# Performance work log

Hardware: AMD Instinct MI355X
Metric: run time of the kernel (lower is better)

The kernel has to match this reference:

```python
import jax, jax.numpy as jnp
import numpy as np

K = 4  # kernel_size

def setup_inputs() -> dict:
    key = jax.random.key(0)
    k1, k2, k3 = jax.random.split(key, 3)
    B, T, C = 4, 4096, 2048
    x = jax.random.normal(k1, (B, T, C), dtype=jnp.float32)
    # depthwise Conv1d weight (C, 1, K) flattened to (C, K); PyTorch default init scale
    bound = 1.0 / np.sqrt(K)
    weight = jax.random.uniform(k2, (C, K), dtype=jnp.float32, minval=-bound, maxval=bound)
    bias = jax.random.uniform(k3, (C,), dtype=jnp.float32, minval=-bound, maxval=bound)
    return {"x": x, "weight": weight, "bias": bias}

def reference(x, weight, bias):
    # Causal depthwise conv on (B,T,C) directly (no transpose needed in jax):
    # y[b,t,c] = sum_k weight[c,k] * x[b, t-(K-1)+k, c] + bias[c]; out = x + y
    B, T, C = x.shape
    xp = jnp.pad(x, ((0, 0), (K - 1, 0), (0, 0)))  # left-pad time axis
    y = bias[None, None, :]
    for k in range(K):  # small fixed kernel taps
        y = y + xp[:, k:k + T, :] * weight[None, None, :, k]
    return x + y
```

## Files before the change

kernel.cpp:

```cpp
#include <hip/hip_runtime.h>

#define B_DIM 4
#define T_DIM 4096
#define C_DIM 2048
#define KK 4
#define C4 (C_DIM / 4)
#define ROWS (B_DIM * T_DIM)
#define NV4 (ROWS * C4)
#define BLOCK 256
#define NBLK 2048
#define NTHREADS (NBLK * BLOCK)
#define ITERS (NV4 / NTHREADS)

typedef float v4f __attribute__((ext_vector_type(4)));

__global__ __launch_bounds__(256) void canonconv_kernel(
    const float* __restrict__ x,
    const float* __restrict__ w,
    const float* __restrict__ bias,
    float* __restrict__ out)
{
    const int tid = blockIdx.x * BLOCK + threadIdx.x;
    const int c4  = tid & (C4 - 1);
    const int c   = c4 * 4;

    const v4f* wv = (const v4f*)(w + (size_t)c * KK);
    const v4f a0 = wv[0];
    const v4f a1 = wv[1];
    const v4f a2 = wv[2];
    const v4f a3 = wv[3];
    const v4f bv = *(const v4f*)(bias + c);

    v4f tap0, tap1, tap2, tap3;
    tap0.x = a0.x; tap0.y = a1.x; tap0.z = a2.x; tap0.w = a3.x;
    tap1.x = a0.y; tap1.y = a1.y; tap1.z = a2.y; tap1.w = a3.y;
    tap2.x = a0.z; tap2.y = a1.z; tap2.z = a2.z; tap2.w = a3.z;
    tap3.x = 1.0f + a0.w; tap3.y = 1.0f + a1.w; tap3.z = 1.0f + a2.w; tap3.w = 1.0f + a3.w;

    const v4f* xv = (const v4f*)x;
    v4f*       ov = (v4f*)out;

    #pragma unroll 1
    for (int iter = 0; iter < ITERS; ++iter) {
        const int p   = tid + iter * NTHREADS;
        const int row = p >> 9;
        const int t   = row & (T_DIM - 1);

        const v4f xc = xv[p];
        v4f xm1 = (v4f)0.0f, xm2 = (v4f)0.0f, xm3 = (v4f)0.0f;
        if (t >= 1) xm1 = xv[p - C4];
        if (t >= 2) xm2 = xv[p - 2 * C4];
        if (t >= 3) xm3 = xv[p - 3 * C4];

        v4f r;
        r.x = fmaf(xc.x, tap3.x, fmaf(xm1.x, tap2.x, fmaf(xm2.x, tap1.x, fmaf(xm3.x, tap0.x, bv.x))));
        r.y = fmaf(xc.y, tap3.y, fmaf(xm1.y, tap2.y, fmaf(xm2.y, tap1.y, fmaf(xm3.y, tap0.y, bv.y))));
        r.z = fmaf(xc.z, tap3.z, fmaf(xm1.z, tap2.z, fmaf(xm2.z, tap1.z, fmaf(xm3.z, tap0.z, bv.z))));
        r.w = fmaf(xc.w, tap3.w, fmaf(xm1.w, tap2.w, fmaf(xm2.w, tap1.w, fmaf(xm3.w, tap0.w, bv.w))));

        ov[p] = r;
    }
}

extern "C" void kernel_launch(void* const* d_in, const int* in_sizes, int n_in,
                              void* d_out, int out_size, void* d_ws, size_t ws_size,
                              hipStream_t stream) {
    const float* x    = (const float*)d_in[0];
    const float* w    = (const float*)d_in[1];
    const float* bias = (const float*)d_in[2];
    float* out = (float*)d_out;

    canonconv_kernel<<<NBLK, BLOCK, 0, stream>>>(x, w, bias, out);
}
```

Baseline: 255.1 us.

## Tile rows per block and reuse previous time steps in registers

Each block now handles 16 consecutive time rows for all 512 channel vectors. Each thread keeps a sliding window of the last three inputs in registers instead of reloading them from global memory. This cuts redundant loads, roughly four reads per output down to one plus a three-row halo per tile, and removes per-element boundary branches. In exchange the grid changes to 1024 blocks of 512 threads with a fully unrolled loop, which raises register use and changes occupancy.

New measurement: 237.0 us. -7.1%, faster.

```diff
diff --git a/kernel.cpp b/kernel.cpp
--- a/kernel.cpp
+++ b/kernel.cpp
@@ -6,23 +6,22 @@
 #define KK 4
 #define C4 (C_DIM / 4)
 #define ROWS (B_DIM * T_DIM)
-#define NV4 (ROWS * C4)
-#define BLOCK 256
-#define NBLK 2048
-#define NTHREADS (NBLK * BLOCK)
-#define ITERS (NV4 / NTHREADS)
+#define BLOCK 512
+#define RR 16
+#define NBLK (ROWS / RR)
 
 typedef float v4f __attribute__((ext_vector_type(4)));
 
-__global__ __launch_bounds__(256) void canonconv_kernel(
+__global__ __launch_bounds__(512) void canonconv_kernel(
     const float* __restrict__ x,
     const float* __restrict__ w,
     const float* __restrict__ bias,
     float* __restrict__ out)
 {
-    const int tid = blockIdx.x * BLOCK + threadIdx.x;
-    const int c4  = tid & (C4 - 1);
-    const int c   = c4 * 4;
+    const int c4   = threadIdx.x;
+    const int row0 = blockIdx.x * RR;
+    const int t0   = row0 & (T_DIM - 1);
+    const int c    = c4 * 4;
 
     const v4f* wv = (const v4f*)(w + (size_t)c * KK);
     const v4f a0 = wv[0];
@@ -37,28 +36,32 @@
     tap2.x = a0.z; tap2.y = a1.z; tap2.z = a2.z; tap2.w = a3.z;
     tap3.x = 1.0f + a0.w; tap3.y = 1.0f + a1.w; tap3.z = 1.0f + a2.w; tap3.w = 1.0f + a3.w;
 
-    const v4f* xv = (const v4f*)x;
-    v4f*       ov = (v4f*)out;
+    const v4f* xp = (const v4f*)x + (size_t)row0 * C4 + c4;
+    v4f*       op = (v4f*)out     + (size_t)row0 * C4 + c4;
 
-    #pragma unroll 1
-    for (int iter = 0; iter < ITERS; ++iter) {
-        const int p   = tid + iter * NTHREADS;
-        const int row = p >> 9;
-        const int t   = row & (T_DIM - 1);
+    v4f xm1, xm2, xm3;
+    if (t0 != 0) {
+        xm3 = xp[-3 * C4];
+        xm2 = xp[-2 * C4];
+        xm1 = xp[-1 * C4];
+    } else {
+        xm3 = (v4f)0.0f;
+        xm2 = (v4f)0.0f;
+        xm1 = (v4f)0.0f;
+    }
 
-        const v4f xc = xv[p];
-        v4f xm1 = (v4f)0.0f, xm2 = (v4f)0.0f, xm3 = (v4f)0.0f;
-        if (t >= 1) xm1 = xv[p - C4];
-        if (t >= 2) xm2 = xv[p - 2 * C4];
-        if (t >= 3) xm3 = xv[p - 3 * C4];
-
+    #pragma unroll
+    for (int j = 0; j < RR; ++j) {
+        const v4f xc = xp[j * C4];
         v4f r;
         r.x = fmaf(xc.x, tap3.x, fmaf(xm1.x, tap2.x, fmaf(xm2.x, tap1.x, fmaf(xm3.x, tap0.x, bv.x))));
         r.y = fmaf(xc.y, tap3.y, fmaf(xm1.y, tap2.y, fmaf(xm2.y, tap1.y, fmaf(xm3.y, tap0.y, bv.y))));
         r.z = fmaf(xc.z, tap3.z, fmaf(xm1.z, tap2.z, fmaf(xm2.z, tap1.z, fmaf(xm3.z, tap0.z, bv.z))));
         r.w = fmaf(xc.w, tap3.w, fmaf(xm1.w, tap2.w, fmaf(xm2.w, tap1.w, fmaf(xm3.w, tap0.w, bv.w))));
-
-        ov[p] = r;
+        op[j * C4] = r;
+        xm3 = xm2;
+        xm2 = xm1;
+        xm1 = xc;
     }
 }
 
```
